# Optimization experiments

Measured on AMD Instinct MI355X. Metric: run time of the kernel, lower is better.

Reference implementation:

```python
import jax, jax.numpy as jnp
import numpy as np

N = 100000      # nodes
D = 128         # embed_dim == hidden_size (code forces them equal)
M = 3           # edge_types / meta-paths
L = 2           # layers
E = 1600000     # edges per meta-path (avg degree 16)
ATT = 128       # semantic attention hidden size


def setup_inputs():
    key = jax.random.key(0)
    ks = jax.random.split(key, 8)
    x = jnp.arange(N)
    edge_index0 = jax.random.randint(ks[0], (2, E), 0, N)
    edge_index1 = jax.random.randint(ks[1], (2, E), 0, N)
    edge_index2 = jax.random.randint(ks[2], (2, E), 0, N)
    embed_table = jax.random.normal(ks[3], (N, D), dtype=jnp.float32) * 0.02
    W = jax.random.normal(ks[4], (L, M, D, D), dtype=jnp.float32) / np.sqrt(D)
    B = jnp.zeros((L, M, D), dtype=jnp.float32)
    att_w1 = jax.random.normal(ks[5], (L, D, ATT), dtype=jnp.float32) / np.sqrt(D)
    att_b1 = jnp.zeros((L, ATT), dtype=jnp.float32)
    att_w2 = jax.random.normal(ks[6], (L, ATT, 1), dtype=jnp.float32) / np.sqrt(ATT)
    return dict(x=x, edge_index0=edge_index0, edge_index1=edge_index1,
                edge_index2=edge_index2, embed_table=embed_table, W=W, B=B,
                att_w1=att_w1, att_b1=att_b1, att_w2=att_w2)


def _gcn_conv(h, W, b, src, dst):
    # GCNConv(normalize=True): self-loops already appended to src/dst.
    deg = jax.ops.segment_sum(jnp.ones_like(dst, dtype=h.dtype), dst, num_segments=N)
    dinv = jnp.where(deg > 0, jax.lax.rsqrt(deg), 0.0)
    norm = dinv[src] * dinv[dst]                       # [E+N]
    hw = h @ W                                         # [N, D]
    msg = hw[src] * norm[:, None]                      # gather + scale
    return jax.ops.segment_sum(msg, dst, num_segments=N) + b


def reference(x, edge_index0, edge_index1, edge_index2,
              embed_table, W, B, att_w1, att_b1, att_w2):
    edges = [edge_index0, edge_index1, edge_index2]
    loops = jnp.arange(N)
    srcs = [jnp.concatenate([e[0], loops]) for e in edges]
    dsts = [jnp.concatenate([e[1], loops]) for e in edges]

    h = embed_table[x]                                 # [N, D]
    for l in range(L):
        sems = [_gcn_conv(h, W[l, m], B[l, m], srcs[m], dsts[m]) for m in range(M)]
        z = jnp.stack(sems, axis=1)                    # [N, M, D]
        # semantic attention: Linear -> tanh -> Linear(no bias), softmax over M
        w = jnp.tanh(z @ att_w1[l] + att_b1[l]) @ att_w2[l]   # [N, M, 1]
        beta = jax.nn.softmax(w, axis=1)
        h = (beta * z).sum(axis=1)                     # [N, D]
    return jax.nn.log_softmax(h, axis=1)
```

## Files before the change

### kernel.cpp

```cpp
#include <hip/hip_runtime.h>
#include <hip/hip_bf16.h>

#define NN 100000
#define DD 128
#define MM 3
#define EE 1600000
#define NBUK ((NN + 127) / 128)
#define CAP 2336
#define CSRTOT ((size_t)NBUK * CAP)
#define TILE_E 8192
#define NTILES ((EE + TILE_E - 1) / TILE_E)
#define HSCALE 64.0f
#define HINV (1.0f / 64.0f)

typedef unsigned int uint32_hip;
typedef short short8 __attribute__((ext_vector_type(8)));
typedef float floatx4 __attribute__((ext_vector_type(4)));
typedef float floatx2 __attribute__((ext_vector_type(2)));

__device__ __forceinline__ float bflo(uint32_hip u) { return __uint_as_float(u << 16); }
__device__ __forceinline__ float bfhi(uint32_hip u) { return __uint_as_float(u & 0xffff0000u); }
__device__ __forceinline__ float bf2f(short s) {
  return __uint_as_float(((uint32_hip)(unsigned short)s) << 16);
}
__device__ __forceinline__ unsigned short f2bf(float f) {
  union { __hip_bfloat16 b; unsigned short u; } cv;
  cv.b = __float2bfloat16(f);
  return cv.u;
}
__device__ __forceinline__ uint32_hip packbf2(float x, float y) {
  return (uint32_hip)f2bf(x) | ((uint32_hip)f2bf(y) << 16);
}
__device__ __forceinline__ float tanh_apx(float x) {
  float e = __expf(2.0f * x);
  return 1.0f - 2.0f / (e + 1.0f);
}
__device__ __forceinline__ uint32_hip pack_fp8x4(float a, float b, float c, float d) {
  uint32_hip w = 0;
  w = __builtin_amdgcn_cvt_pk_fp8_f32(a, b, w, false);
  w = __builtin_amdgcn_cvt_pk_fp8_f32(c, d, w, true);
  return w;
}
__device__ __forceinline__ float h2f(uint32_hip u) {
  union { unsigned short us; _Float16 h; } cv;
  cv.us = (unsigned short)u;
  return (float)cv.h;
}
__device__ __forceinline__ unsigned short f2h(float f) {
  union { unsigned short us; _Float16 h; } cv;
  cv.h = (_Float16)f;
  return cv.us;
}
__device__ __forceinline__ void dec8(uint2 hv, float* f) {
  floatx2 p0 = __builtin_amdgcn_cvt_pk_f32_fp8((int)hv.x, false);
  floatx2 p1 = __builtin_amdgcn_cvt_pk_f32_fp8((int)hv.x, true);
  floatx2 p2 = __builtin_amdgcn_cvt_pk_f32_fp8((int)hv.y, false);
  floatx2 p3 = __builtin_amdgcn_cvt_pk_f32_fp8((int)hv.y, true);
  f[0] = p0.x; f[1] = p0.y; f[2] = p1.x; f[3] = p1.y;
  f[4] = p2.x; f[5] = p2.y; f[6] = p3.x; f[7] = p3.y;
}

__global__ void init_bcur_kernel(int* __restrict__ bcur) {
  int i = blockIdx.x * 256 + threadIdx.x;
  if (i < MM * NBUK) bcur[i] = (i % NBUK) * CAP;
}

__global__ void partition_kernel(const int* __restrict__ e0, const int* __restrict__ e1,
                                 const int* __restrict__ e2, int* __restrict__ bcur,
                                 uint32_hip* __restrict__ ebuf) {
  __shared__ int hist[NBUK];
  int m = blockIdx.y, t = threadIdx.x;
  const int* ei = (m == 0) ? e0 : (m == 1) ? e1 : e2;
  const int* dst = ei + EE;
  int beg = blockIdx.x * TILE_E, end = min(beg + TILE_E, EE);
  for (int b = t; b < NBUK; b += 256) hist[b] = 0;
  __syncthreads();
  for (int e = beg + t; e < end; e += 256) atomicAdd(&hist[dst[e] >> 7], 1);
  __syncthreads();
  for (int b = t; b < NBUK; b += 256) {
    int c = hist[b];
    hist[b] = c ? atomicAdd(&bcur[m * NBUK + b], c) : 0;
  }
  __syncthreads();
  uint32_hip* eb = ebuf + (size_t)m * CSRTOT;
  for (int e = beg + t; e < end; e += 256) {
    int d = dst[e];
    int pos = atomicAdd(&hist[d >> 7], 1);
    eb[pos] = (uint32_hip)ei[e] | ((uint32_hip)(d & 127) << 17);
  }
}

__global__ void bucket_sort_kernel(uint32_hip* __restrict__ ebuf, const int* __restrict__ bcur,
                                   int* __restrict__ astart, unsigned short* __restrict__ sdeg) {
  __shared__ uint32_hip ebl[CAP];
  __shared__ int cnt[128];
  __shared__ int pos[128];
  int m = blockIdx.y, b = blockIdx.x, t = threadIdx.x;
  int base = b * CAP;
  int ct = bcur[m * NBUK + b] - base;
  uint32_hip* eb = ebuf + (size_t)m * CSRTOT + base;
  for (int e = t; e < ct; e += 256) ebl[e] = eb[e];
  if (t < 128) cnt[t] = 0;
  __syncthreads();
  for (int e = t; e < ct; e += 256) atomicAdd(&cnt[ebl[e] >> 17], 1);
  __syncthreads();
  if (t < 128) pos[t] = cnt[t];
  __syncthreads();
  for (int off = 1; off < 128; off <<= 1) {
    int v = (t < 128 && t >= off) ? pos[t - off] : 0;
    __syncthreads();
    if (t < 128) pos[t] += v;
    __syncthreads();
  }
  int node0 = b * 128;
  if (t < 128) {
    int excl = pos[t] - cnt[t];
    pos[t] = excl;
    int node = node0 + t;
    if (node < NN) {
      astart[(size_t)m * NN + node] = base + excl;
      sdeg[(size_t)m * NN + node] = (unsigned short)cnt[t];
    }
  }
  __syncthreads();
  for (int e = t; e < ct; e += 256) {
    uint32_hip p = ebl[e];
    int q = atomicAdd(&pos[p >> 17], 1);
    eb[q] = p & 0x1FFFFu;
  }
}

__global__ void norm_embed_kernel(uint32_hip* __restrict__ ebuf, const int* __restrict__ bcur,
                                  const unsigned short* __restrict__ sdeg) {
  int m = blockIdx.y, b = blockIdx.x, t = threadIdx.x;
  int base = b * CAP;
  int ct = bcur[m * NBUK + b] - base;
  uint32_hip* eb = ebuf + (size_t)m * CSRTOT + base;
  const unsigned short* sd = sdeg + (size_t)m * NN;
  for (int e = t; e < ct; e += 256) {
    uint32_hip s = eb[e] & 0x1FFFFu;
    float dv = rsqrtf((float)(sd[s] + 1));
    eb[e] = s | ((uint32_hip)f2h(dv) << 17);
  }
}

__global__ void embed_kernel(const int* __restrict__ x, const float* __restrict__ tbl,
                             uint32_hip* __restrict__ hq) {
  int i = blockIdx.x * 256 + threadIdx.x;
  if (i < NN * 32) {
    int n = i >> 5;
    int c = i & 31;
    float4 v = ((const float4*)tbl)[(size_t)x[n] * 32 + c];
    hq[(size_t)n * 32 + c] =
        pack_fp8x4(v.x * HSCALE, v.y * HSCALE, v.z * HSCALE, v.w * HSCALE);
  }
}

__global__ __launch_bounds__(256) void agg_kernel(const uint32_hip* __restrict__ hq,
                                                  const unsigned short* __restrict__ sdeg,
                                                  const int* __restrict__ astart,
                                                  const uint32_hip* __restrict__ csr,
                                                  uint32_hip* __restrict__ zall) {
  int m = blockIdx.y;
  const unsigned short* sd = sdeg + (size_t)m * NN;
  const int* as_ = astart + (size_t)m * NN;
  const uint32_hip* cs = csr + (size_t)m * CSRTOT;
  uint32_hip* zo = zall + (size_t)m * NN * 64;
  int t = threadIdx.x;
  int wave = t >> 6, lane = t & 63;
  int g = lane >> 4, l = lane & 15;
  int n = blockIdx.x * 16 + wave * 4 + g;
  int deg = sd[n];
  float di = rsqrtf((float)(deg + 1));

  float ac[8];
  {
    uint2 hv = *(const uint2*)(hq + (size_t)n * 32 + l * 2);
    float f[8];
    dec8(hv, f);
#pragma unroll
    for (int j = 0; j < 8; ++j) ac[j] = di * f[j];
  }

  int e = as_[n];
  int end = e + deg;
  bool v0 = e < end, v1 = (e + 1) < end;
  uint32_hip c0 = cs[v0 ? e : 0];
  uint32_hip c1 = cs[v1 ? e + 1 : 0];
  while (__any(v0)) {
    int en = e + 2;
    bool u0 = en < end, u1 = (en + 1) < end;
    uint32_hip d0 = cs[u0 ? en : 0];
    uint32_hip d1 = cs[u1 ? en + 1 : 0];
    float n0 = v0 ? h2f(c0 >> 17) : 0.f;
    float n1 = v1 ? h2f(c1 >> 17) : 0.f;
    int s0 = c0 & 0x1FFFF, s1 = c1 & 0x1FFFF;
    uint2 h0 = *(const uint2*)(hq + (size_t)s0 * 32 + l * 2);
    uint2 h1 = *(const uint2*)(hq + (size_t)s1 * 32 + l * 2);
    float f0[8], f1[8];
    dec8(h0, f0);
    dec8(h1, f1);
#pragma unroll
    for (int j = 0; j < 8; ++j) ac[j] = fmaf(n0, f0[j], ac[j]);
#pragma unroll
    for (int j = 0; j < 8; ++j) ac[j] = fmaf(n1, f1[j], ac[j]);
    e = en;
    v0 = u0;
    v1 = u1;
    c0 = d0;
    c1 = d1;
  }

  float sc = di * HINV;
  uint4 w;
  w.x = packbf2(ac[0] * sc, ac[1] * sc);
  w.y = packbf2(ac[2] * sc, ac[3] * sc);
  w.z = packbf2(ac[4] * sc, ac[5] * sc);
  w.w = packbf2(ac[6] * sc, ac[7] * sc);
  *(uint4*)(zo + (size_t)n * 64 + l * 4) = w;
}

__global__ __launch_bounds__(256) void mfma_gemm_kernel(unsigned short* __restrict__ zall,
                                                        const float* __restrict__ Wall,
                                                        const float* __restrict__ Ball) {
  __shared__ unsigned short Wt[128 * 136];
  int m = blockIdx.y;
  const float* Wmat = Wall + (size_t)m * DD * DD;
  const float* bias = Ball + (size_t)m * DD;
  unsigned short* Z = zall + (size_t)m * NN * DD;
  int t = threadIdx.x;
  {
    uint32_hip* Wt_u = (uint32_hip*)Wt;
#pragma unroll
    for (int i = 0; i < 32; ++i) {
      int idx = i * 256 + t;
      int k2 = idx >> 7;
      int nn = idx & 127;
      float w0 = Wmat[(2 * k2) * 128 + nn];
      float w1 = Wmat[(2 * k2 + 1) * 128 + nn];
      Wt_u[nn * 68 + k2] = packbf2(w0, w1);
    }
  }
  __syncthreads();
  int wave = t >> 6, lane = t & 63;
  int quad = lane >> 4, ln = lane & 15;
  int rowbase = blockIdx.x * 64 + wave * 16;
  int arow = rowbase + ln;
  int arowc = (arow < NN) ? arow : (NN - 1);
  const short8* zrow = (const short8*)(Z + (size_t)arowc * 128);
  floatx4 acc[8];
#pragma unroll
  for (int c = 0; c < 8; ++c) acc[c] = (floatx4){0.f, 0.f, 0.f, 0.f};
#pragma unroll
  for (int kt = 0; kt < 4; ++kt) {
    short8 a = zrow[kt * 4 + quad];
#pragma unroll
    for (int c = 0; c < 8; ++c) {
      const short8* bp = (const short8*)(Wt + (c * 16 + ln) * 136 + kt * 32 + quad * 8);
      acc[c] = __builtin_amdgcn_mfma_f32_16x16x32_bf16(a, *bp, acc[c], 0, 0, 0);
    }
  }
#pragma unroll
  for (int c = 0; c < 8; ++c) {
    int col = c * 16 + ln;
    float bs = bias[col];
#pragma unroll
    for (int r = 0; r < 4; ++r) {
      int grow = rowbase + quad * 4 + r;
      if (grow < NN) Z[(size_t)grow * 128 + col] = f2bf(acc[c][r] + bs);
    }
  }
}

__global__ __launch_bounds__(256) void att_combine_kernel(
    const unsigned short* __restrict__ Z, const float* __restrict__ W1,
    const float* __restrict__ b1, const float* __restrict__ w2,
    uint32_hip* __restrict__ hq, float* __restrict__ fout, int last) {
  __shared__ unsigned short Wt[128 * 136];
  __shared__ float sc[4][3][16];
  int t = threadIdx.x;
  {
    uint32_hip* Wt_u = (uint32_hip*)Wt;
#pragma unroll
    for (int i = 0; i < 32; ++i) {
      int idx = i * 256 + t;
      int k2 = idx >> 7;
      int nn = idx & 127;
      float w0 = W1[(2 * k2) * 128 + nn];
      float w1 = W1[(2 * k2 + 1) * 128 + nn];
      Wt_u[nn * 68 + k2] = packbf2(w0, w1);
    }
  }
  __syncthreads();
  int wave = t >> 6, lane = t & 63;
  int quad = lane >> 4, ln = lane & 15;
  int nodebase = blockIdx.x * 64 + wave * 16;
  int frow = nodebase + ln;
  int frowc = (frow < NN) ? frow : (NN - 1);
  short8 af[3][4];
#pragma unroll
  for (int m = 0; m < 3; ++m) {
    const short8* zr = (const short8*)(Z + ((size_t)m * NN + frowc) * 128);
#pragma unroll
    for (int kt = 0; kt < 4; ++kt) af[m][kt] = zr[kt * 4 + quad];
  }
#pragma unroll
  for (int m = 0; m < 3; ++m) {
    floatx4 acc[8];
#pragma unroll
    for (int c = 0; c < 8; ++c) acc[c] = (floatx4){0.f, 0.f, 0.f, 0.f};
#pragma unroll
    for (int kt = 0; kt < 4; ++kt) {
#pragma unroll
      for (int c = 0; c < 8; ++c) {
        const short8* bp = (const short8*)(Wt + (c * 16 + ln) * 136 + kt * 32 + quad * 8);
        acc[c] = __builtin_amdgcn_mfma_f32_16x16x32_bf16(af[m][kt], *bp, acc[c], 0, 0, 0);
      }
    }
    float rows[4] = {0.f, 0.f, 0.f, 0.f};
#pragma unroll
    for (int c = 0; c < 8; ++c) {
      int col = c * 16 + ln;
      float bb = b1[col];
      float ww = w2[col];
#pragma unroll
      for (int r = 0; r < 4; ++r) rows[r] += tanh_apx(acc[c][r] + bb) * ww;
    }
#pragma unroll
    for (int off = 8; off > 0; off >>= 1) {
#pragma unroll
      for (int r = 0; r < 4; ++r) rows[r] += __shfl_down(rows[r], off);
    }
    if (ln == 0) {
#pragma unroll
      for (int r = 0; r < 4; ++r) sc[wave][m][quad * 4 + r] = rows[r];
    }
  }
  __syncthreads();
  float s0 = sc[wave][0][ln], s1 = sc[wave][1][ln], s2 = sc[wave][2][ln];
  float mx = fmaxf(s0, fmaxf(s1, s2));
  float e0 = __expf(s0 - mx), e1 = __expf(s1 - mx), e2 = __expf(s2 - mx);
  float inv = 1.0f / (e0 + e1 + e2);
  float bb0 = e0 * inv, bb1 = e1 * inv, bb2 = e2 * inv;
  float o[4][8];
#pragma unroll
  for (int kt = 0; kt < 4; ++kt) {
#pragma unroll
    for (int j = 0; j < 8; ++j) {
      o[kt][j] = bb0 * bf2f(af[0][kt][j]) + bb1 * bf2f(af[1][kt][j]) + bb2 * bf2f(af[2][kt][j]);
    }
  }
  if (!last) {
    if (frow < NN) {
#pragma unroll
      for (int kt = 0; kt < 4; ++kt) {
        uint2 v;
        v.x = pack_fp8x4(o[kt][0] * HSCALE, o[kt][1] * HSCALE, o[kt][2] * HSCALE,
                         o[kt][3] * HSCALE);
        v.y = pack_fp8x4(o[kt][4] * HSCALE, o[kt][5] * HSCALE, o[kt][6] * HSCALE,
                         o[kt][7] * HSCALE);
        *(uint2*)&hq[(size_t)frow * 32 + kt * 8 + quad * 2] = v;
      }
    }
  } else {
    float vmx = o[0][0];
#pragma unroll
    for (int kt = 0; kt < 4; ++kt)
#pragma unroll
      for (int j = 0; j < 8; ++j) vmx = fmaxf(vmx, o[kt][j]);
    vmx = fmaxf(vmx, __shfl_xor(vmx, 16));
    vmx = fmaxf(vmx, __shfl_xor(vmx, 32));
    float ss = 0.f;
#pragma unroll
    for (int kt = 0; kt < 4; ++kt)
#pragma unroll
      for (int j = 0; j < 8; ++j) ss += __expf(o[kt][j] - vmx);
    ss += __shfl_xor(ss, 16);
    ss += __shfl_xor(ss, 32);
    float lse = vmx + logf(ss);
    if (frow < NN) {
#pragma unroll
      for (int kt = 0; kt < 4; ++kt) {
        float4 a, b;
        a.x = o[kt][0] - lse; a.y = o[kt][1] - lse; a.z = o[kt][2] - lse; a.w = o[kt][3] - lse;
        b.x = o[kt][4] - lse; b.y = o[kt][5] - lse; b.z = o[kt][6] - lse; b.w = o[kt][7] - lse;
        float* dst = fout + (size_t)frow * 128 + kt * 32 + quad * 8;
        *(float4*)dst = a;
        *(float4*)(dst + 4) = b;
      }
    }
  }
}

extern "C" void kernel_launch(void* const* d_in, const int* in_sizes, int n_in,
                              void* d_out, int out_size, void* d_ws, size_t ws_size,
                              hipStream_t stream) {
  const int* x = (const int*)d_in[0];
  const int* e0 = (const int*)d_in[1];
  const int* e1 = (const int*)d_in[2];
  const int* e2 = (const int*)d_in[3];
  const float* embed = (const float*)d_in[4];
  const float* W = (const float*)d_in[5];
  const float* B = (const float*)d_in[6];
  const float* aw1 = (const float*)d_in[7];
  const float* ab1 = (const float*)d_in[8];
  const float* aw2 = (const float*)d_in[9];
  float* out = (float*)d_out;
  uint32_hip* hq = (uint32_hip*)d_out;

  char* ws = (char*)d_ws;
  size_t off = 0;
  auto alloc = [&](size_t bytes) {
    void* p = ws + off;
    off += (bytes + 255) & ~(size_t)255;
    return p;
  };
  unsigned short* z = (unsigned short*)alloc((size_t)MM * NN * DD * 2);
  uint32_hip* ebuf = (uint32_hip*)alloc((size_t)MM * CSRTOT * 4);
  int* astart = (int*)alloc((size_t)MM * NN * 4);
  unsigned short* sdeg = (unsigned short*)alloc((size_t)MM * NN * 2);
  int* bcur = (int*)alloc((size_t)MM * NBUK * 4);

  dim3 bs(256);
  init_bcur_kernel<<<dim3((MM * NBUK + 255) / 256), bs, 0, stream>>>(bcur);
  partition_kernel<<<dim3(NTILES, 3), bs, 0, stream>>>(e0, e1, e2, bcur, ebuf);
  bucket_sort_kernel<<<dim3(NBUK, 3), bs, 0, stream>>>(ebuf, bcur, astart, sdeg);
  norm_embed_kernel<<<dim3(NBUK, 3), bs, 0, stream>>>(ebuf, bcur, sdeg);
  embed_kernel<<<dim3((NN * 32 + 255) / 256), bs, 0, stream>>>(x, embed, hq);

  for (int l = 0; l < 2; ++l) {
    agg_kernel<<<dim3((NN + 15) / 16, 3), bs, 0, stream>>>(
        (const uint32_hip*)hq, sdeg, astart, ebuf, (uint32_hip*)z);
    mfma_gemm_kernel<<<dim3((NN + 63) / 64, 3), bs, 0, stream>>>(
        z, W + (size_t)l * 3 * DD * DD, B + (size_t)l * 3 * DD);
    att_combine_kernel<<<dim3((NN + 63) / 64), bs, 0, stream>>>(
        z, aw1 + (size_t)l * DD * DD, ab1 + (size_t)l * DD, aw2 + (size_t)l * DD, hq, out, l == 1);
  }
}
```

Measured before the change: 705.3 us.

## Replace atomic bucket partition with histogram, scan, scatter passes

The edge partition step used a single kernel that reserved bucket space with global atomics on a shared cursor array. It now runs three kernels: per-tile bucket histograms written to a tile-by-bucket table, a per-bucket exclusive scan over tiles, and a scatter that uses the scanned offsets. The tile size also drops from 8192 to 2048 edges, so there are more blocks. This removes global atomic contention and makes the bucket layout deterministic, at the cost of reading the destination indices twice, one extra launch, and a large histogram table to write and read.

Result: slower. 733.0 us (+3.9%).

```diff
diff --git a/kernel.cpp b/kernel.cpp
--- a/kernel.cpp
+++ b/kernel.cpp
@@ -8,8 +8,9 @@
 #define NBUK ((NN + 127) / 128)
 #define CAP 2336
 #define CSRTOT ((size_t)NBUK * CAP)
-#define TILE_E 8192
+#define TILE_E 2048
 #define NTILES ((EE + TILE_E - 1) / TILE_E)
+#define TH_PITCH 784
 #define HSCALE 64.0f
 #define HINV (1.0f / 64.0f)
 
@@ -18,8 +19,6 @@
 typedef float floatx4 __attribute__((ext_vector_type(4)));
 typedef float floatx2 __attribute__((ext_vector_type(2)));
 
-__device__ __forceinline__ float bflo(uint32_hip u) { return __uint_as_float(u << 16); }
-__device__ __forceinline__ float bfhi(uint32_hip u) { return __uint_as_float(u & 0xffff0000u); }
 __device__ __forceinline__ float bf2f(short s) {
   return __uint_as_float(((uint32_hip)(unsigned short)s) << 16);
 }
@@ -60,32 +59,71 @@
   f[4] = p2.x; f[5] = p2.y; f[6] = p3.x; f[7] = p3.y;
 }
 
-__global__ void init_bcur_kernel(int* __restrict__ bcur) {
-  int i = blockIdx.x * 256 + threadIdx.x;
-  if (i < MM * NBUK) bcur[i] = (i % NBUK) * CAP;
-}
-
-__global__ void partition_kernel(const int* __restrict__ e0, const int* __restrict__ e1,
-                                 const int* __restrict__ e2, int* __restrict__ bcur,
-                                 uint32_hip* __restrict__ ebuf) {
+__global__ __launch_bounds__(256) void hist_kernel(const int* __restrict__ e0,
+                                                   const int* __restrict__ e1,
+                                                   const int* __restrict__ e2,
+                                                   int* __restrict__ thist) {
   __shared__ int hist[NBUK];
-  int m = blockIdx.y, t = threadIdx.x;
+  int m = blockIdx.y, tile = blockIdx.x, t = threadIdx.x;
   const int* ei = (m == 0) ? e0 : (m == 1) ? e1 : e2;
   const int* dst = ei + EE;
-  int beg = blockIdx.x * TILE_E, end = min(beg + TILE_E, EE);
+  int beg = tile * TILE_E, end = min(beg + TILE_E, EE);
   for (int b = t; b < NBUK; b += 256) hist[b] = 0;
   __syncthreads();
   for (int e = beg + t; e < end; e += 256) atomicAdd(&hist[dst[e] >> 7], 1);
   __syncthreads();
-  for (int b = t; b < NBUK; b += 256) {
-    int c = hist[b];
-    hist[b] = c ? atomicAdd(&bcur[m * NBUK + b], c) : 0;
-  }
+  int* th = thist + (size_t)m * NBUK * TH_PITCH + tile;
+  for (int b = t; b < NBUK; b += 256) th[(size_t)b * TH_PITCH] = hist[b];
+}
+
+__global__ __launch_bounds__(256) void scan_kernel(int* __restrict__ thist,
+                                                   int* __restrict__ bcur) {
+  __shared__ int sw[256];
+  int b = blockIdx.x, m = blockIdx.y, t = threadIdx.x;
+  int* th = thist + ((size_t)m * NBUK + b) * TH_PITCH;
+  int v[4];
+  int s = 0;
+#pragma unroll
+  for (int j = 0; j < 4; ++j) {
+    int tt = t * 4 + j;
+    v[j] = (tt < NTILES) ? th[tt] : 0;
+    s += v[j];
+  }
+  sw[t] = s;
+  __syncthreads();
+  for (int off = 1; off < 256; off <<= 1) {
+    int u = (t >= off) ? sw[t - off] : 0;
+    __syncthreads();
+    sw[t] += u;
+    __syncthreads();
+  }
+  int base = b * CAP + sw[t] - s;
+#pragma unroll
+  for (int j = 0; j < 4; ++j) {
+    int tt = t * 4 + j;
+    if (tt < NTILES) th[tt] = base;
+    base += v[j];
+  }
+  if (t == 255) bcur[m * NBUK + b] = b * CAP + sw[255];
+}
+
+__global__ __launch_bounds__(256) void scatter_kernel(const int* __restrict__ e0,
+                                                      const int* __restrict__ e1,
+                                                      const int* __restrict__ e2,
+                                                      const int* __restrict__ thist,
+                                                      uint32_hip* __restrict__ ebuf) {
+  __shared__ int cur[NBUK];
+  int m = blockIdx.y, tile = blockIdx.x, t = threadIdx.x;
+  const int* ei = (m == 0) ? e0 : (m == 1) ? e1 : e2;
+  const int* dst = ei + EE;
+  int beg = tile * TILE_E, end = min(beg + TILE_E, EE);
+  const int* th = thist + (size_t)m * NBUK * TH_PITCH + tile;
+  for (int b = t; b < NBUK; b += 256) cur[b] = th[(size_t)b * TH_PITCH];
   __syncthreads();
   uint32_hip* eb = ebuf + (size_t)m * CSRTOT;
   for (int e = beg + t; e < end; e += 256) {
     int d = dst[e];
-    int pos = atomicAdd(&hist[d >> 7], 1);
+    int pos = atomicAdd(&cur[d >> 7], 1);
     eb[pos] = (uint32_hip)ei[e] | ((uint32_hip)(d & 127) << 17);
   }
 }
@@ -420,10 +458,12 @@
   int* astart = (int*)alloc((size_t)MM * NN * 4);
   unsigned short* sdeg = (unsigned short*)alloc((size_t)MM * NN * 2);
   int* bcur = (int*)alloc((size_t)MM * NBUK * 4);
+  int* thist = (int*)alloc((size_t)MM * NBUK * TH_PITCH * 4);
 
   dim3 bs(256);
-  init_bcur_kernel<<<dim3((MM * NBUK + 255) / 256), bs, 0, stream>>>(bcur);
-  partition_kernel<<<dim3(NTILES, 3), bs, 0, stream>>>(e0, e1, e2, bcur, ebuf);
+  hist_kernel<<<dim3(NTILES, 3), bs, 0, stream>>>(e0, e1, e2, thist);
+  scan_kernel<<<dim3(NBUK, 3), bs, 0, stream>>>(thist, bcur);
+  scatter_kernel<<<dim3(NTILES, 3), bs, 0, stream>>>(e0, e1, e2, thist, ebuf);
   bucket_sort_kernel<<<dim3(NBUK, 3), bs, 0, stream>>>(ebuf, bcur, astart, sdeg);
   norm_embed_kernel<<<dim3(NBUK, 3), bs, 0, stream>>>(ebuf, bcur, sdeg);
   embed_kernel<<<dim3((NN * 32 + 255) / 256), bs, 0, stream>>>(x, embed, hq);
```
